# Kernel tuning notes

Hardware: AMD Instinct MI355X
Metric: run time of the kernel (lower is better)

Reference implementation:

```python
import jax, jax.numpy as jnp
import numpy as np

V_IN = 32000
V_OUT = 32000
E = 1024
H = 1024
B = 16
T = 512


def _lstm_layer(xs, Wih, Whh, bih, bhh):
    # xs: [T, B, in_dim]; PyTorch gate order: i, f, g, o (each size H)
    gx = jnp.einsum('tbi,gi->tbg', xs, Wih) + bih + bhh  # [T, B, 4H]

    def step(carry, g_t):
        h, c = carry
        g = g_t + h @ Whh.T  # [B, 4H]
        i, f, gg, o = jnp.split(g, 4, axis=-1)
        i = jax.nn.sigmoid(i)
        f = jax.nn.sigmoid(f)
        gg = jnp.tanh(gg)
        o = jax.nn.sigmoid(o)
        c = f * c + i * gg
        h = o * jnp.tanh(c)
        return (h, c), h

    h0 = jnp.zeros((xs.shape[1], Whh.shape[1]), dtype=xs.dtype)
    c0 = jnp.zeros_like(h0)
    _, hs = jax.lax.scan(step, (h0, c0), gx)
    return hs  # [T, B, H]


def setup_inputs() -> dict:
    key = jax.random.key(0)
    ks = jax.random.split(key, 12)
    s_e = 1.0  # nn.Embedding default init is N(0,1)
    s_l = 1.0 / np.sqrt(H)  # LSTM/Linear uniform bound 1/sqrt(H)

    def u(k, shape):
        return jax.random.uniform(k, shape, jnp.float32, -s_l, s_l)

    return {
        'x': jax.random.randint(ks[0], (B, T), 0, V_IN),
        'emb': jax.random.normal(ks[1], (V_IN, E), jnp.float32) * s_e,
        'W_ih0': u(ks[2], (4 * H, E)),
        'W_hh0': u(ks[3], (4 * H, H)),
        'b_ih0': u(ks[4], (4 * H,)),
        'b_hh0': u(ks[5], (4 * H,)),
        'W_ih1': u(ks[6], (4 * H, H)),
        'W_hh1': u(ks[7], (4 * H, H)),
        'b_ih1': u(ks[8], (4 * H,)),
        'b_hh1': u(ks[9], (4 * H,)),
        'W_out': u(ks[10], (V_OUT, H)),
        'b_out': u(ks[11], (V_OUT,)),
    }


def reference(x, emb, W_ih0, W_hh0, b_ih0, b_hh0, W_ih1, W_hh1, b_ih1, b_hh1, W_out, b_out):
    # embedding + permute to [T, B, E]
    out = emb[x].transpose(1, 0, 2)
    out = _lstm_layer(out, W_ih0, W_hh0, b_ih0, b_hh0)
    out = _lstm_layer(out, W_ih1, W_hh1, b_ih1, b_hh1)
    logits = jnp.einsum('tbh,oh->tbo', out, W_out) + b_out
    return logits.transpose(1, 0, 2)  # [B, T, V_OUT]
```

## Files before the change

### kernel.cpp

```cpp
#include <hip/hip_runtime.h>
#include <cstdint>
#include <cstddef>

typedef __bf16 bf16;
typedef float f32x4 __attribute__((ext_vector_type(4)));
typedef bf16 bf16x8 __attribute__((ext_vector_type(8)));
typedef bf16 bf16x4 __attribute__((ext_vector_type(4)));

#define AS1 __attribute__((address_space(1)))
#define AS3 __attribute__((address_space(3)))

__device__ __forceinline__ void gload_lds16(const void* g, void* l) {
  __builtin_amdgcn_global_load_lds((AS1 void*)g, (AS3 void*)l, 16, 0, 0);
}

#define NBLK_W 192
#define FSTR 32
#define FLAG_WORDS ((64 + 128 + 192 + 128) * FSTR)

__global__ __launch_bounds__(256) void init_misc(
    const float* __restrict__ bih0, const float* __restrict__ bhh0,
    const float* __restrict__ bih1, const float* __restrict__ bhh1,
    float* __restrict__ bsum0, float* __restrict__ bsum1, unsigned* __restrict__ flags) {
  int i = blockIdx.x * 256 + threadIdx.x;
  if (i < 4096) {
    bsum0[i] = bih0[i] + bhh0[i];
    bsum1[i] = bih1[i] + bhh1[i];
  }
  if (i < FLAG_WORDS) flags[i] = 0u;
}

__global__ __launch_bounds__(256) void embed_gather(
    const int* __restrict__ x, const float* __restrict__ emb, bf16* __restrict__ xe, int T) {
  int row = blockIdx.x;
  int t = row >> 4, b = row & 15;
  int tok = x[b * T + t];
  int cix = threadIdx.x << 2;
  f32x4 v = *(const f32x4*)(emb + ((size_t)tok << 10) + cix);
  bf16x4 o;
  for (int j = 0; j < 4; ++j) o[j] = (bf16)v[j];
  *(bf16x4*)(xe + ((size_t)row << 10) + cix) = o;
}

template <int OUTMODE>
__global__ __launch_bounds__(256) void gemm_bf16(
    const bf16* __restrict__ A, const float* __restrict__ Bw,
    const float* __restrict__ bias, float* __restrict__ C,
    int M, int N, int K, int Tdim) {
  __shared__ bf16 aL[2][128 * 32];
  __shared__ bf16 bL[2][128 * 32];
  const int tid = threadIdx.x;
  const int l = tid & 63, w = tid >> 6;
  const int nbm = M >> 7;
  const int bm = blockIdx.x % nbm;
  const int bn = blockIdx.x / nbm;
  const int wr = (w >> 1) << 6, wc = (w & 1) << 6;
  const int NT = K >> 5;
  const int r16 = l & 15, kq = l >> 4;

  f32x4 acc[4][4];
  for (int m = 0; m < 4; ++m)
    for (int n = 0; n < 4; ++n) acc[m][n] = (f32x4){0.f, 0.f, 0.f, 0.f};

  for (int i = 0; i < 2; ++i) {
    int lin = tid + (i << 8);
    int r = lin >> 2, s = lin & 3, c = s ^ (r & 3);
    gload_lds16(A + (size_t)((bm << 7) + r) * K + (c << 3), &aL[0][lin << 3]);
  }
  for (int i = 0; i < 2; ++i) {
    int lin = tid + (i << 8);
    int r = lin >> 2, c = lin & 3;
    const float* src = Bw + (size_t)((bn << 7) + r) * K + (c << 3);
    f32x4 v0 = *(const f32x4*)src;
    f32x4 v1 = *(const f32x4*)(src + 4);
    bf16x8 o;
    for (int j = 0; j < 4; ++j) { o[j] = (bf16)v0[j]; o[j + 4] = (bf16)v1[j]; }
    *(bf16x8*)&bL[0][(r << 5) + ((c ^ (r & 3)) << 3)] = o;
  }
  __syncthreads();

  for (int kt = 0; kt < NT; ++kt) {
    const int cur = kt & 1;
    const bool pf = (kt + 1 < NT);
    f32x4 bv0[2], bv1[2];
    int br_[2], bs_[2];
    if (pf) {
      for (int i = 0; i < 2; ++i) {
        int lin = tid + (i << 8);
        int r = lin >> 2, s = lin & 3, c = s ^ (r & 3);
        gload_lds16(A + (size_t)((bm << 7) + r) * K + ((kt + 1) << 5) + (c << 3),
                    &aL[cur ^ 1][lin << 3]);
      }
      for (int i = 0; i < 2; ++i) {
        int lin = tid + (i << 8);
        int r = lin >> 2, c = lin & 3;
        const float* src = Bw + (size_t)((bn << 7) + r) * K + ((kt + 1) << 5) + (c << 3);
        bv0[i] = *(const f32x4*)src;
        bv1[i] = *(const f32x4*)(src + 4);
        br_[i] = r;
        bs_[i] = c ^ (r & 3);
      }
    }
    bf16x8 af[4], bfr[4];
    for (int m = 0; m < 4; ++m) {
      int row = wr + (m << 4) + r16;
      int ch = kq ^ (row & 3);
      af[m] = *(const bf16x8*)&aL[cur][(row << 5) + (ch << 3)];
    }
    for (int n = 0; n < 4; ++n) {
      int row = wc + (n << 4) + r16;
      int ch = kq ^ (row & 3);
      bfr[n] = *(const bf16x8*)&bL[cur][(row << 5) + (ch << 3)];
    }
    for (int m = 0; m < 4; ++m)
      for (int n = 0; n < 4; ++n)
        acc[m][n] = __builtin_amdgcn_mfma_f32_16x16x32_bf16(af[m], bfr[n], acc[m][n], 0, 0, 0);
    if (pf) {
      for (int i = 0; i < 2; ++i) {
        bf16x8 o;
        for (int j = 0; j < 4; ++j) { o[j] = (bf16)bv0[i][j]; o[j + 4] = (bf16)bv1[i][j]; }
        *(bf16x8*)&bL[cur ^ 1][(br_[i] << 5) + (bs_[i] << 3)] = o;
      }
    }
    __syncthreads();
  }

  float bvv[4];
  for (int n = 0; n < 4; ++n) bvv[n] = bias[(bn << 7) + wc + (n << 4) + r16];
  for (int m = 0; m < 4; ++m) {
    int Rbase = (bm << 7) + wr + (m << 4) + (kq << 2);
    for (int r = 0; r < 4; ++r) {
      int R = Rbase + r;
      size_t rowoff;
      if (OUTMODE == 0) {
        rowoff = (size_t)R * N;
      } else {
        int tt = R >> 4, bb = R & 15;
        rowoff = ((size_t)bb * Tdim + tt) * N;
      }
      for (int n = 0; n < 4; ++n)
        C[rowoff + (bn << 7) + wc + (n << 4) + r16] = acc[m][n][r] + bvv[n];
    }
  }
}

__global__ __launch_bounds__(256, 1) void lstm_pipe(
    const float* __restrict__ gx,
    const float* __restrict__ Whh0,
    const float* __restrict__ Wih1,
    const float* __restrict__ Whh1,
    const float* __restrict__ bsum1,
    bf16* __restrict__ hs0,
    bf16* __restrict__ hs1,
    unsigned* __restrict__ flags,
    int T) {
  __shared__ bf16 wlds[64 * 1024];
  __shared__ float glds[4 * 16 * 16];
  const int tid = threadIdx.x;
  const int l = tid & 63, w = tid >> 6;
  const int bid = blockIdx.x;
  unsigned* const flag0 = flags;
  unsigned* const flag1 = flags + 64 * FSTR;
  unsigned* const mbA = flags + 192 * FSTR;
  unsigned* const mbB = flags + 384 * FSTR;

  if (bid == NBLK_W) {
    if (w == 0) {
      unsigned* fp = flag0 + (size_t)l * FSTR;
      unsigned* m0 = mbA + (size_t)l * FSTR;
      unsigned* m1 = mbA + (size_t)(l + 64) * FSTR;
      unsigned* m2 = mbA + (size_t)(l + 128) * FSTR;
      for (int e = 1; e <= T; ++e) {
        while (__hip_atomic_load(fp, __ATOMIC_RELAXED, __HIP_MEMORY_SCOPE_AGENT) < (unsigned)e) {
        }
        __hip_atomic_store(m0, (unsigned)e, __ATOMIC_RELAXED, __HIP_MEMORY_SCOPE_AGENT);
        __hip_atomic_store(m1, (unsigned)e, __ATOMIC_RELAXED, __HIP_MEMORY_SCOPE_AGENT);
        __hip_atomic_store(m2, (unsigned)e, __ATOMIC_RELAXED, __HIP_MEMORY_SCOPE_AGENT);
      }
    } else if (w == 1) {
      unsigned* fa = flag1 + (size_t)l * FSTR;
      unsigned* fb = flag1 + (size_t)(l + 64) * FSTR;
      unsigned* m0 = mbB + (size_t)l * FSTR;
      unsigned* m1 = mbB + (size_t)(l + 64) * FSTR;
      for (int e = 1; e <= T - 1; ++e) {
        while (__hip_atomic_load(fa, __ATOMIC_RELAXED, __HIP_MEMORY_SCOPE_AGENT) < (unsigned)e) {
        }
        while (__hip_atomic_load(fb, __ATOMIC_RELAXED, __HIP_MEMORY_SCOPE_AGENT) < (unsigned)e) {
        }
        __hip_atomic_store(m0, (unsigned)e, __ATOMIC_RELAXED, __HIP_MEMORY_SCOPE_AGENT);
        __hip_atomic_store(m1, (unsigned)e, __ATOMIC_RELAXED, __HIP_MEMORY_SCOPE_AGENT);
      }
    }
    return;
  }

  const bool L0 = bid < 64;
  const int r16 = l & 15, kq = l >> 4, rx = r16 & 7;

  if (L0) {
    const int j0s = bid << 4;
    for (int it = 0; it < 32; ++it) {
      int lin = tid + (it << 8);
      int row = lin >> 7, cs = lin & 127, c = cs ^ (row & 7);
      int g = row >> 4, n = row & 15;
      const float* src = Whh0 + (size_t)(g * 1024 + j0s + n) * 1024 + (c << 3);
      f32x4 v0 = *(const f32x4*)src;
      f32x4 v1 = *(const f32x4*)(src + 4);
      bf16x8 o;
      for (int j = 0; j < 4; ++j) { o[j] = (bf16)v0[j]; o[j + 4] = (bf16)v1[j]; }
      *(bf16x8*)(wlds + (row << 10) + (cs << 3)) = o;
    }
  } else {
    const int j0s = (bid - 64) << 3;
    for (int it = 0; it < 32; ++it) {
      int lin = tid + (it << 8);
      int row = lin >> 7, cs = lin & 127, c = cs ^ (row & 7);
      int m = row >> 5, rr = row & 31, g = rr >> 3, n = rr & 7;
      const float* W = m ? Whh1 : Wih1;
      const float* src = W + (size_t)(g * 1024 + j0s + n) * 1024 + (c << 3);
      f32x4 v0 = *(const f32x4*)src;
      f32x4 v1 = *(const f32x4*)(src + 4);
      bf16x8 o;
      for (int j = 0; j < 4; ++j) { o[j] = (bf16)v0[j]; o[j + 4] = (bf16)v1[j]; }
      *(bf16x8*)(wlds + (row << 10) + (cs << 3)) = o;
    }
  }
  __syncthreads();

  if (L0) {
    const int j0 = bid << 4;
    const int bidx = tid >> 4, jl = tid & 15;
    unsigned* const myflag = flag0 + (size_t)bid * FSTR;
    unsigned* const mymb = mbA + (size_t)bid * FSTR;
    float cst = 0.f;

    for (int t = 0; t < T; ++t) {
      const float* gp = gx + ((((size_t)t << 4) + bidx) << 12) + j0 + jl;
      float gi = gp[0], gf = gp[1024], gg2 = gp[2048], go_ = gp[3072];
      if (t > 0 && tid == 0) {
        while (__hip_atomic_load(mymb, __ATOMIC_RELAXED, __HIP_MEMORY_SCOPE_AGENT) < (unsigned)t) {
        }
      }
      __syncthreads();
      asm volatile("" ::: "memory");

      f32x4 acc = (f32x4){0.f, 0.f, 0.f, 0.f};
      f32x4 acc2 = (f32x4){0.f, 0.f, 0.f, 0.f};
      if (t > 0) {
        const bf16* hp = hs0 + ((size_t)(t - 1) << 14) + (r16 << 10) + (kq << 3);
        const bf16* wb = wlds + (((w << 4) + r16) << 10);
#pragma unroll 8
        for (int kk = 0; kk < 32; kk += 2) {
          bf16x8 a0 = *(const bf16x8*)(hp + (kk << 5));
          bf16x8 a1 = *(const bf16x8*)(hp + ((kk + 1) << 5));
          acc = __builtin_amdgcn_mfma_f32_16x16x32_bf16(
              a0, *(const bf16x8*)(wb + ((((kk << 2) + kq) ^ rx) << 3)), acc, 0, 0, 0);
          acc2 = __builtin_amdgcn_mfma_f32_16x16x32_bf16(
              a1, *(const bf16x8*)(wb + (((((kk + 1) << 2) + kq) ^ rx) << 3)), acc2, 0, 0, 0);
        }
      }
      for (int r = 0; r < 4; ++r)
        glds[(w << 8) + (((kq << 2) + r) << 4) + r16] = acc[r] + acc2[r];
      __syncthreads();

      float xi = glds[(bidx << 4) + jl] + gi;
      float xf = glds[256 + (bidx << 4) + jl] + gf;
      float xg = glds[512 + (bidx << 4) + jl] + gg2;
      float xo = glds[768 + (bidx << 4) + jl] + go_;
      float ig = 1.f / (1.f + __expf(-xi));
      float fg = 1.f / (1.f + __expf(-xf));
      float eg = __expf(2.f * xg);
      float ggv = 1.f - 2.f / (eg + 1.f);
      float og = 1.f / (1.f + __expf(-xo));
      cst = fg * cst + ig * ggv;
      float ec = __expf(2.f * cst);
      float th = 1.f - 2.f / (ec + 1.f);
      bf16 hb = (bf16)(og * th);
      unsigned hu = (unsigned)__builtin_bit_cast(unsigned short, hb);
      unsigned other = (unsigned)__shfl_xor((int)hu, 1, 64);
      if (!(tid & 1)) {
        unsigned pair = (hu & 0xffffu) | (other << 16);
        bf16* sp = hs0 + ((((size_t)t << 4) + bidx) << 10) + j0 + jl;
        asm volatile("global_store_dword %0, %1, off sc1 nt" ::"v"(sp), "v"(pair) : "memory");
      }
      asm volatile("s_waitcnt vmcnt(0)" ::: "memory");
      __syncthreads();
      if (tid == 0)
        __hip_atomic_store(myflag, (unsigned)(t + 1), __ATOMIC_RELAXED, __HIP_MEMORY_SCOPE_AGENT);
    }
  } else {
    const int j0 = (bid - 64) << 3;
    const int b1 = tid >> 3, j1 = tid & 7;
    unsigned* const myflag = flag1 + (size_t)(bid - 64) * FSTR;
    unsigned* const mbAp = mbA + (size_t)bid * FSTR;
    unsigned* const mbBp = mbB + (size_t)(bid - 64) * FSTR;
    float cst = 0.f;
    float bi_ = 0.f, bf_ = 0.f, bg_ = 0.f, bo_ = 0.f;
    if (tid < 128) {
      bi_ = bsum1[j0 + j1];
      bf_ = bsum1[1024 + j0 + j1];
      bg_ = bsum1[2048 + j0 + j1];
      bo_ = bsum1[3072 + j0 + j1];
    }

    for (int t1 = 0; t1 < T; ++t1) {
      if (tid < 2) {
        unsigned tgt = (tid == 0) ? (unsigned)(t1 + 1) : (unsigned)t1;
        unsigned* wp = (tid == 0) ? mbAp : mbBp;
        while (tgt &&
               __hip_atomic_load(wp, __ATOMIC_RELAXED, __HIP_MEMORY_SCOPE_AGENT) < tgt) {
        }
      }
      __syncthreads();
      asm volatile("" ::: "memory");

      f32x4 acc0 = (f32x4){0.f, 0.f, 0.f, 0.f};
      f32x4 acc1 = (f32x4){0.f, 0.f, 0.f, 0.f};
      const bf16* hp0 = hs0 + ((size_t)t1 << 14) + (r16 << 10) + (kq << 3);
      const bf16* wb0 = wlds + (((w << 3) + rx) << 10);
      const bf16* wb1 = wlds + ((32 + (w << 3) + rx) << 10);
#pragma unroll 8
      for (int kk = 0; kk < 32; ++kk) {
        bf16x8 a0 = *(const bf16x8*)(hp0 + (kk << 5));
        acc0 = __builtin_amdgcn_mfma_f32_16x16x32_bf16(
            a0, *(const bf16x8*)(wb0 + ((((kk << 2) + kq) ^ rx) << 3)), acc0, 0, 0, 0);
      }
      if (t1 > 0) {
        const bf16* hp1 = hs1 + ((size_t)(t1 - 1) << 14) + (r16 << 10) + (kq << 3);
#pragma unroll 8
        for (int kk = 0; kk < 32; ++kk) {
          bf16x8 a1 = *(const bf16x8*)(hp1 + (kk << 5));
          acc1 = __builtin_amdgcn_mfma_f32_16x16x32_bf16(
              a1, *(const bf16x8*)(wb1 + ((((kk << 2) + kq) ^ rx) << 3)), acc1, 0, 0, 0);
        }
      }
      for (int r = 0; r < 4; ++r)
        glds[(w << 8) + (((kq << 2) + r) << 4) + r16] = acc0[r] + acc1[r];
      __syncthreads();

      if (tid < 128) {
        float xi = glds[(b1 << 4) + j1] + bi_;
        float xf = glds[256 + (b1 << 4) + j1] + bf_;
        float xg = glds[512 + (b1 << 4) + j1] + bg_;
        float xo = glds[768 + (b1 << 4) + j1] + bo_;
        float ig = 1.f / (1.f + __expf(-xi));
        float fg = 1.f / (1.f + __expf(-xf));
        float eg = __expf(2.f * xg);
        float ggv = 1.f - 2.f / (eg + 1.f);
        float og = 1.f / (1.f + __expf(-xo));
        cst = fg * cst + ig * ggv;
        float ec = __expf(2.f * cst);
        float th = 1.f - 2.f / (ec + 1.f);
        bf16 hb = (bf16)(og * th);
        unsigned hu = (unsigned)__builtin_bit_cast(unsigned short, hb);
        unsigned other = (unsigned)__shfl_xor((int)hu, 1, 64);
        if (!(tid & 1)) {
          unsigned pair = (hu & 0xffffu) | (other << 16);
          bf16* sp = hs1 + ((((size_t)t1 << 4) + b1) << 10) + j0 + j1;
          asm volatile("global_store_dword %0, %1, off sc1 nt" ::"v"(sp), "v"(pair) : "memory");
        }
      }
      asm volatile("s_waitcnt vmcnt(0)" ::: "memory");
      __syncthreads();
      if (tid == 0)
        __hip_atomic_store(myflag, (unsigned)(t1 + 1), __ATOMIC_RELAXED, __HIP_MEMORY_SCOPE_AGENT);
    }
  }
}

extern "C" void kernel_launch(void* const* d_in, const int* in_sizes, int n_in,
                              void* d_out, int out_size, void* d_ws, size_t ws_size,
                              hipStream_t stream) {
  const int* x = (const int*)d_in[0];
  const float* emb = (const float*)d_in[1];
  const float* Wih0 = (const float*)d_in[2];
  const float* Whh0 = (const float*)d_in[3];
  const float* bih0 = (const float*)d_in[4];
  const float* bhh0 = (const float*)d_in[5];
  const float* Wih1 = (const float*)d_in[6];
  const float* Whh1 = (const float*)d_in[7];
  const float* bih1 = (const float*)d_in[8];
  const float* bhh1 = (const float*)d_in[9];
  const float* Wout = (const float*)d_in[10];
  const float* bout = (const float*)d_in[11];

  const int T = 512, H = 1024, V = 32000;
  const int M = T * 16;
  const size_t bfb = (size_t)M * H * 2;

  char* p = (char*)d_ws;
  bf16* hs1 = (bf16*)p;           p += bfb;
  float* bsum0 = (float*)p;       p += 4096 * 4;
  float* bsum1 = (float*)p;       p += 4096 * 4;
  unsigned* flags = (unsigned*)p; p += FLAG_WORDS * 4;
  size_t base_need = (size_t)(p - (char*)d_ws);
  bf16 *xe, *hs0;
  if (ws_size >= base_need + 2 * bfb) {
    xe = (bf16*)p;
    hs0 = (bf16*)(p + bfb);
  } else {
    char* tail = (char*)d_out + (size_t)out_size * 4 - 2 * bfb;
    xe = (bf16*)tail;
    hs0 = (bf16*)(tail + bfb);
  }
  float* gx = (float*)d_out;

  init_misc<<<64, 256, 0, stream>>>(bih0, bhh0, bih1, bhh1, bsum0, bsum1, flags);
  embed_gather<<<M, 256, 0, stream>>>(x, emb, xe, T);
  gemm_bf16<0><<<(M / 128) * (4096 / 128), 256, 0, stream>>>(xe, Wih0, bsum0, gx, M, 4096, H, 0);
  lstm_pipe<<<NBLK_W + 1, 256, 0, stream>>>(gx, Whh0, Wih1, Whh1, bsum1, hs0, hs1, flags, T);
  gemm_bf16<1><<<(M / 128) * (V / 128), 256, 0, stream>>>(hs1, Wout, bout, (float*)d_out, M, V, H, T);
}
```

Baseline: 6.183 ms.

## Replace relay-block barrier with direct per-consumer flag matrices in LSTM pipeline

Removes the dedicated relay block that collected per-block completion flags and rebroadcast them to mailboxes. Each producer block now writes its step counter directly into a consumer-indexed flag matrix, and each consumer waits with a full wavefront polling 64 or 128 flags in parallel. This drops one hop of global-memory latency from every recurrent step. The cost is more flag memory and more stores per step. The hidden-state stores also drop the nt hint.

```diff
diff --git a/kernel.cpp b/kernel.cpp
--- a/kernel.cpp
+++ b/kernel.cpp
@@ -15,8 +15,10 @@
 }
 
 #define NBLK_W 192
-#define FSTR 32
-#define FLAG_WORDS ((64 + 128 + 192 + 128) * FSTR)
+#define D0_WORDS (64 * 64)
+#define D01_WORDS (128 * 64)
+#define D1_WORDS (128 * 128)
+#define FLAG_WORDS (D0_WORDS + D01_WORDS + D1_WORDS)
 
 __global__ __launch_bounds__(256) void init_misc(
     const float* __restrict__ bih0, const float* __restrict__ bhh0,
@@ -27,7 +29,7 @@
     bsum0[i] = bih0[i] + bhh0[i];
     bsum1[i] = bih1[i] + bhh1[i];
   }
-  if (i < FLAG_WORDS) flags[i] = 0u;
+  for (int k = i; k < FLAG_WORDS; k += 64 * 256) flags[k] = 0u;
 }
 
 __global__ __launch_bounds__(256) void embed_gather(
@@ -159,40 +161,9 @@
   const int tid = threadIdx.x;
   const int l = tid & 63, w = tid >> 6;
   const int bid = blockIdx.x;
-  unsigned* const flag0 = flags;
-  unsigned* const flag1 = flags + 64 * FSTR;
-  unsigned* const mbA = flags + 192 * FSTR;
-  unsigned* const mbB = flags + 384 * FSTR;
-
-  if (bid == NBLK_W) {
-    if (w == 0) {
-      unsigned* fp = flag0 + (size_t)l * FSTR;
-      unsigned* m0 = mbA + (size_t)l * FSTR;
-      unsigned* m1 = mbA + (size_t)(l + 64) * FSTR;
-      unsigned* m2 = mbA + (size_t)(l + 128) * FSTR;
-      for (int e = 1; e <= T; ++e) {
-        while (__hip_atomic_load(fp, __ATOMIC_RELAXED, __HIP_MEMORY_SCOPE_AGENT) < (unsigned)e) {
-        }
-        __hip_atomic_store(m0, (unsigned)e, __ATOMIC_RELAXED, __HIP_MEMORY_SCOPE_AGENT);
-        __hip_atomic_store(m1, (unsigned)e, __ATOMIC_RELAXED, __HIP_MEMORY_SCOPE_AGENT);
-        __hip_atomic_store(m2, (unsigned)e, __ATOMIC_RELAXED, __HIP_MEMORY_SCOPE_AGENT);
-      }
-    } else if (w == 1) {
-      unsigned* fa = flag1 + (size_t)l * FSTR;
-      unsigned* fb = flag1 + (size_t)(l + 64) * FSTR;
-      unsigned* m0 = mbB + (size_t)l * FSTR;
-      unsigned* m1 = mbB + (size_t)(l + 64) * FSTR;
-      for (int e = 1; e <= T - 1; ++e) {
-        while (__hip_atomic_load(fa, __ATOMIC_RELAXED, __HIP_MEMORY_SCOPE_AGENT) < (unsigned)e) {
-        }
-        while (__hip_atomic_load(fb, __ATOMIC_RELAXED, __HIP_MEMORY_SCOPE_AGENT) < (unsigned)e) {
-        }
-        __hip_atomic_store(m0, (unsigned)e, __ATOMIC_RELAXED, __HIP_MEMORY_SCOPE_AGENT);
-        __hip_atomic_store(m1, (unsigned)e, __ATOMIC_RELAXED, __HIP_MEMORY_SCOPE_AGENT);
-      }
-    }
-    return;
-  }
+  unsigned* const done0 = flags;
+  unsigned* const done01 = flags + D0_WORDS;
+  unsigned* const done1 = flags + D0_WORDS + D01_WORDS;
 
   const bool L0 = bid < 64;
   const int r16 = l & 15, kq = l >> 4, rx = r16 & 7;
@@ -230,15 +201,15 @@
   if (L0) {
     const int j0 = bid << 4;
     const int bidx = tid >> 4, jl = tid & 15;
-    unsigned* const myflag = flag0 + (size_t)bid * FSTR;
-    unsigned* const mymb = mbA + (size_t)bid * FSTR;
     float cst = 0.f;
 
     for (int t = 0; t < T; ++t) {
       const float* gp = gx + ((((size_t)t << 4) + bidx) << 12) + j0 + jl;
       float gi = gp[0], gf = gp[1024], gg2 = gp[2048], go_ = gp[3072];
-      if (t > 0 && tid == 0) {
-        while (__hip_atomic_load(mymb, __ATOMIC_RELAXED, __HIP_MEMORY_SCOPE_AGENT) < (unsigned)t) {
+      if (t > 0 && w == 0) {
+        const unsigned* fp = done0 + (bid << 6) + l;
+        while (__hip_atomic_load(fp, __ATOMIC_RELAXED, __HIP_MEMORY_SCOPE_AGENT) <
+               (unsigned)t) {
         }
       }
       __syncthreads();
@@ -281,19 +252,26 @@
       if (!(tid & 1)) {
         unsigned pair = (hu & 0xffffu) | (other << 16);
         bf16* sp = hs0 + ((((size_t)t << 4) + bidx) << 10) + j0 + jl;
-        asm volatile("global_store_dword %0, %1, off sc1 nt" ::"v"(sp), "v"(pair) : "memory");
+        asm volatile("global_store_dword %0, %1, off sc1" ::"v"(sp), "v"(pair) : "memory");
       }
       asm volatile("s_waitcnt vmcnt(0)" ::: "memory");
       __syncthreads();
-      if (tid == 0)
-        __hip_atomic_store(myflag, (unsigned)(t + 1), __ATOMIC_RELAXED, __HIP_MEMORY_SCOPE_AGENT);
+
+      const unsigned ep = (unsigned)(t + 1);
+      if (w == 0)
+        __hip_atomic_store(done0 + (l << 6) + bid, ep, __ATOMIC_RELAXED,
+                           __HIP_MEMORY_SCOPE_AGENT);
+      else if (w == 1)
+        __hip_atomic_store(done01 + (l << 6) + bid, ep, __ATOMIC_RELAXED,
+                           __HIP_MEMORY_SCOPE_AGENT);
+      else if (w == 2)
+        __hip_atomic_store(done01 + ((64 + l) << 6) + bid, ep, __ATOMIC_RELAXED,
+                           __HIP_MEMORY_SCOPE_AGENT);
     }
   } else {
-    const int j0 = (bid - 64) << 3;
+    const int q = bid - 64;
+    const int j0 = q << 3;
     const int b1 = tid >> 3, j1 = tid & 7;
-    unsigned* const myflag = flag1 + (size_t)(bid - 64) * FSTR;
-    unsigned* const mbAp = mbA + (size_t)bid * FSTR;
-    unsigned* const mbBp = mbB + (size_t)(bid - 64) * FSTR;
     float cst = 0.f;
     float bi_ = 0.f, bf_ = 0.f, bg_ = 0.f, bo_ = 0.f;
     if (tid < 128) {
@@ -304,11 +282,20 @@
     }
 
     for (int t1 = 0; t1 < T; ++t1) {
-      if (tid < 2) {
-        unsigned tgt = (tid == 0) ? (unsigned)(t1 + 1) : (unsigned)t1;
-        unsigned* wp = (tid == 0) ? mbAp : mbBp;
-        while (tgt &&
-               __hip_atomic_load(wp, __ATOMIC_RELAXED, __HIP_MEMORY_SCOPE_AGENT) < tgt) {
+      if (w == 0) {
+        const unsigned* fp = done01 + (q << 6) + l;
+        while (__hip_atomic_load(fp, __ATOMIC_RELAXED, __HIP_MEMORY_SCOPE_AGENT) <
+               (unsigned)(t1 + 1)) {
+        }
+      } else if (w == 1 && t1 > 0) {
+        const unsigned* fp = done1 + (q << 7) + l;
+        while (__hip_atomic_load(fp, __ATOMIC_RELAXED, __HIP_MEMORY_SCOPE_AGENT) <
+               (unsigned)t1) {
+        }
+      } else if (w == 2 && t1 > 0) {
+        const unsigned* fp = done1 + (q << 7) + 64 + l;
+        while (__hip_atomic_load(fp, __ATOMIC_RELAXED, __HIP_MEMORY_SCOPE_AGENT) <
+               (unsigned)t1) {
         }
       }
       __syncthreads();
@@ -357,13 +344,19 @@
         if (!(tid & 1)) {
           unsigned pair = (hu & 0xffffu) | (other << 16);
           bf16* sp = hs1 + ((((size_t)t1 << 4) + b1) << 10) + j0 + j1;
-          asm volatile("global_store_dword %0, %1, off sc1 nt" ::"v"(sp), "v"(pair) : "memory");
+          asm volatile("global_store_dword %0, %1, off sc1" ::"v"(sp), "v"(pair) : "memory");
         }
       }
       asm volatile("s_waitcnt vmcnt(0)" ::: "memory");
       __syncthreads();
-      if (tid == 0)
-        __hip_atomic_store(myflag, (unsigned)(t1 + 1), __ATOMIC_RELAXED, __HIP_MEMORY_SCOPE_AGENT);
+
+      const unsigned ep = (unsigned)(t1 + 1);
+      if (w == 0)
+        __hip_atomic_store(done1 + (l << 7) + q, ep, __ATOMIC_RELAXED,
+                           __HIP_MEMORY_SCOPE_AGENT);
+      else if (w == 1)
+        __hip_atomic_store(done1 + ((64 + l) << 7) + q, ep, __ATOMIC_RELAXED,
+                           __HIP_MEMORY_SCOPE_AGENT);
     }
   }
 }
@@ -408,6 +401,6 @@
   init_misc<<<64, 256, 0, stream>>>(bih0, bhh0, bih1, bhh1, bsum0, bsum1, flags);
   embed_gather<<<M, 256, 0, stream>>>(x, emb, xe, T);
   gemm_bf16<0><<<(M / 128) * (4096 / 128), 256, 0, stream>>>(xe, Wih0, bsum0, gx, M, 4096, H, 0);
-  lstm_pipe<<<NBLK_W + 1, 256, 0, stream>>>(gx, Whh0, Wih1, Whh1, bsum1, hs0, hs1, flags, T);
+  lstm_pipe<<<NBLK_W, 256, 0, stream>>>(gx, Whh0, Wih1, Whh1, bsum1, hs0, hs1, flags, T);
   gemm_bf16<1><<<(M / 128) * (V / 128), 256, 0, stream>>>(hs1, Wout, bout, (float*)d_out, M, V, H, T);
 }
```

Result: faster. 5.997 ms (-3.0%).
